# Performance work log

Measured on AMD Instinct MI355X. Metric: run time of the kernel, lower is better.

The kernel has to match this reference:

```python
import jax, jax.numpy as jnp
import numpy as np

T, B, H, D = 128, 8, 8, 64


def setup_inputs() -> dict:
    key = jax.random.key(0)
    kA, kB, kS = jax.random.split(key, 3)
    # Gated-delta transition matrices: near-identity contractions so the
    # length-T matrix-product recurrence is numerically stable, mimicking
    # A_t = gamma_t * (I - beta_t k_t k_t^T) of the gated delta rule.
    eye = jnp.eye(D, dtype=jnp.float32)
    A = 0.9 * eye + 0.06 * jax.random.normal(kA, (T, B, H, D, D), dtype=jnp.float32)
    Bm = jax.random.normal(kB, (T, B, H, D, D), dtype=jnp.float32)
    init_state = jax.random.normal(kS, (B, H, D, D), dtype=jnp.float32)
    return {"A": A, "Bm": Bm, "init_state": init_state}


def reference(A, Bm, init_state):
    """Gated delta rule recurrence S_t = S_{t-1} @ A_t + B_t for all t,
    computed with a parallel associative scan (Blelloch-equivalent).

    A:  [T,B,H,D,D] transition matrices
    Bm: [T,B,H,D,D] additive updates
    init_state: [B,H,D,D]
    returns states: [T,B,H,D,D]
    """
    def combine(e1, e2):
        # apply e1 first, then e2:
        # (S A1 + B1) A2 + B2 = S (A1 A2) + (B1 A2 + B2)
        A1, B1 = e1
        A2, B2 = e2
        A12 = jnp.einsum('tbhij,tbhjk->tbhik', A1, A2)
        B12 = jnp.einsum('tbhij,tbhjk->tbhik', B1, A2) + B2
        return (A12, B12)

    cumA, cumB = jax.lax.associative_scan(combine, (A, Bm), axis=0)
    # S_t = init_state @ cumA_t + cumB_t
    states = jnp.einsum('bhij,tbhjk->tbhik', init_state, cumA) + cumB
    return states
```

## Files before the change

kernel.cpp:

```cpp
#include <hip/hip_runtime.h>


constexpr int kT = 128;
constexpr int kBH = 64;
constexpr int kD = 64;
constexpr int kTile = kD * kD;
constexpr int kNC = 16;
constexpr int kCH = 8;

typedef __attribute__((ext_vector_type(8))) short short8;
typedef __attribute__((ext_vector_type(4))) float f32x4;
using u32 = unsigned int;

union U8 { u32 u[4]; short8 s; };

__device__ __forceinline__ void softBarrier() {
  asm volatile("s_waitcnt lgkmcnt(0)" ::: "memory");
  __builtin_amdgcn_s_barrier();
}

__device__ __forceinline__ int swzi(int r, int c) { return (r * 64 + c) ^ ((r & 7) << 3); }

__device__ __forceinline__ f32x4 mfma16(short8 a, short8 b, f32x4 c) {
  return __builtin_amdgcn_mfma_f32_16x16x32_bf16(a, b, c, 0, 0, 0);
}

__device__ __forceinline__ void pk_split(float a, float b, u32& h, u32& l) {
  u32 hu;
  asm("v_cvt_pk_bf16_f32 %0, %1, %2" : "=v"(hu) : "v"(a), "v"(b));
  const float ra = a - __uint_as_float(hu << 16);
  const float rb = b - __uint_as_float(hu & 0xffff0000u);
  u32 lu;
  asm("v_cvt_pk_bf16_f32 %0, %1, %2" : "=v"(lu) : "v"(ra), "v"(rb));
  h = hu;
  l = lu;
}

__device__ __forceinline__ short8 gather_frag(u32 p01, u32 p23, u32 q01, u32 q23,
                                              int ad0, int ad1, bool lowh) {
  U8 r;
  int x, y;
  x = __builtin_amdgcn_ds_bpermute(ad0, (int)p01);
  y = __builtin_amdgcn_ds_bpermute(ad0, (int)q01);
  r.u[0] = (u32)(lowh ? x : y);
  x = __builtin_amdgcn_ds_bpermute(ad0, (int)p23);
  y = __builtin_amdgcn_ds_bpermute(ad0, (int)q23);
  r.u[1] = (u32)(lowh ? x : y);
  x = __builtin_amdgcn_ds_bpermute(ad1, (int)p01);
  y = __builtin_amdgcn_ds_bpermute(ad1, (int)q01);
  r.u[2] = (u32)(lowh ? x : y);
  x = __builtin_amdgcn_ds_bpermute(ad1, (int)p23);
  y = __builtin_amdgcn_ds_bpermute(ad1, (int)q23);
  r.u[3] = (u32)(lowh ? x : y);
  return r.s;
}

__device__ __forceinline__ void load_pfA(float* pfA, const float* At, int lane, int w) {
#pragma unroll
  for (int kk = 0; kk < 16; ++kk) pfA[kk] = At[(w * 16 + kk) * 64 + lane];
}
__device__ __forceinline__ void load_pfB(f32x4* pfB, const float* Bt, int rowbase, int q) {
#pragma unroll
  for (int cm = 0; cm < 4; ++cm)
    pfB[cm] = *reinterpret_cast<const f32x4*>(Bt + rowbase + cm * 16 + q * 4);
}

__device__ __forceinline__ void stage_A(unsigned short* Ah, unsigned short* Al,
                                        const float* pfA, int lane, int w) {
#pragma unroll
  for (int s = 0; s < 2; ++s) {
    U8 h, l;
#pragma unroll
    for (int p = 0; p < 4; ++p) {
      u32 hu, lu;
      pk_split(pfA[s * 8 + 2 * p], pfA[s * 8 + 2 * p + 1], hu, lu);
      h.u[p] = hu;
      l.u[p] = lu;
    }
    const int idx = swzi(lane, w * 16 + s * 8);
    *reinterpret_cast<short8*>(&Ah[idx]) = h.s;
    *reinterpret_cast<short8*>(&Al[idx]) = l.s;
  }
}

__global__ __launch_bounds__(256, 4) void gdr_fold(
    const float* __restrict__ srcA, const float* __restrict__ srcB,
    float* __restrict__ dstA, float* __restrict__ dstB,
    int perChain, long chainBase, long idxBase, long elemStride, int nElem) {
  __shared__ unsigned short sAh[2][4096], sAl[2][4096];

  const int tid = threadIdx.x;
  const int lane = tid & 63, w = tid >> 6;
  const int q = lane >> 4, l15 = lane & 15;
  const int bh = blockIdx.x / perChain, id = blockIdx.x % perChain;
  const long e0 = (long)bh * chainBase + (long)id * idxBase;
  const int rowbase = (w * 16 + l15) * 64;
  const int ad0 = (l15 + ((lane >> 4) & 1) * 32) * 4;
  const int ad1 = ad0 + 64;
  const bool lowh = lane < 32;
  const int nS = nElem - 1;

  f32x4 apa[4], apb[4];
  {
    const float* At = srcA + (size_t)e0 * kTile;
    const float* Bt = srcB + (size_t)e0 * kTile;
#pragma unroll
    for (int cm = 0; cm < 4; ++cm) {
      apa[cm] = *reinterpret_cast<const f32x4*>(At + rowbase + cm * 16 + q * 4);
      apb[cm] = *reinterpret_cast<const f32x4*>(Bt + rowbase + cm * 16 + q * 4);
    }
  }

  float pfA[16];
  f32x4 pfB[4];
  load_pfA(pfA, srcA + (size_t)(e0 + elemStride) * kTile, lane, w);
  stage_A(sAh[0], sAl[0], pfA, lane, w);
  softBarrier();
  {
    const long e2 = e0 + (long)(nS > 1 ? 2 : 1) * elemStride;
    load_pfA(pfA, srcA + (size_t)e2 * kTile, lane, w);
    load_pfB(pfB, srcB + (size_t)(e0 + elemStride) * kTile, rowbase, q);
  }

  for (int j = 0; j < nS; ++j) {
    const int cur = j & 1;
    f32x4 npa[4], npb[4];
#pragma unroll
    for (int cm = 0; cm < 4; ++cm) {
      npa[cm] = (f32x4){0.f, 0.f, 0.f, 0.f};
      npb[cm] = pfB[cm];
    }
#pragma unroll
    for (int ks = 0; ks < 2; ++ks) {
      u32 pa01h, pa01l, pa23h, pa23l, qa01h, qa01l, qa23h, qa23l;
      u32 pb01h, pb01l, pb23h, pb23l, qb01h, qb01l, qb23h, qb23l;
      pk_split(apa[2 * ks][0], apa[2 * ks][1], pa01h, pa01l);
      pk_split(apa[2 * ks][2], apa[2 * ks][3], pa23h, pa23l);
      pk_split(apa[2 * ks + 1][0], apa[2 * ks + 1][1], qa01h, qa01l);
      pk_split(apa[2 * ks + 1][2], apa[2 * ks + 1][3], qa23h, qa23l);
      pk_split(apb[2 * ks][0], apb[2 * ks][1], pb01h, pb01l);
      pk_split(apb[2 * ks][2], apb[2 * ks][3], pb23h, pb23l);
      pk_split(apb[2 * ks + 1][0], apb[2 * ks + 1][1], qb01h, qb01l);
      pk_split(apb[2 * ks + 1][2], apb[2 * ks + 1][3], qb23h, qb23l);
      const short8 bah = gather_frag(pa01h, pa23h, qa01h, qa23h, ad0, ad1, lowh);
      const short8 bal = gather_frag(pa01l, pa23l, qa01l, qa23l, ad0, ad1, lowh);
      const short8 bbh = gather_frag(pb01h, pb23h, qb01h, qb23h, ad0, ad1, lowh);
      const short8 bbl = gather_frag(pb01l, pb23l, qb01l, qb23l, ad0, ad1, lowh);
#pragma unroll
      for (int cm = 0; cm < 4; ++cm) {
        const int ai = swzi(cm * 16 + l15, ks * 32 + q * 8);
        const short8 ah = *reinterpret_cast<const short8*>(&sAh[cur][ai]);
        const short8 al = *reinterpret_cast<const short8*>(&sAl[cur][ai]);
        npa[cm] = mfma16(ah, bah, npa[cm]);
        npa[cm] = mfma16(ah, bal, npa[cm]);
        npa[cm] = mfma16(al, bah, npa[cm]);
        npb[cm] = mfma16(ah, bbh, npb[cm]);
        npb[cm] = mfma16(ah, bbl, npb[cm]);
        npb[cm] = mfma16(al, bbh, npb[cm]);
      }
    }
    if (j + 1 < nS) {
      stage_A(sAh[cur ^ 1], sAl[cur ^ 1], pfA, lane, w);
      const int ja = (j + 3 <= nS) ? j + 3 : nS;
      load_pfA(pfA, srcA + (size_t)(e0 + (long)ja * elemStride) * kTile, lane, w);
      load_pfB(pfB, srcB + (size_t)(e0 + (long)(j + 2) * elemStride) * kTile, rowbase, q);
    }
#pragma unroll
    for (int cm = 0; cm < 4; ++cm) { apa[cm] = npa[cm]; apb[cm] = npb[cm]; }
    if (j + 1 < nS) softBarrier();
  }

  float* pao = dstA + (size_t)blockIdx.x * kTile;
  float* pbo = dstB + (size_t)blockIdx.x * kTile;
#pragma unroll
  for (int cm = 0; cm < 4; ++cm) {
    *reinterpret_cast<f32x4*>(pao + rowbase + cm * 16 + q * 4) = apa[cm];
    *reinterpret_cast<f32x4*>(pbo + rowbase + cm * 16 + q * 4) = apb[cm];
  }
}

__global__ __launch_bounds__(256, 4) void gdr_scan(
    const float* __restrict__ srcA, const float* __restrict__ srcB,
    const float* __restrict__ S0, float* __restrict__ out,
    int perChain, long chainBase, long idxBase, long elemStride,
    int nSteps, int tbMul, int tStep) {
  __shared__ unsigned short sAh[2][4096], sAl[2][4096];

  const int tid = threadIdx.x;
  const int lane = tid & 63, w = tid >> 6;
  const int q = lane >> 4, l15 = lane & 15;
  const int bh = blockIdx.x / perChain, id = blockIdx.x % perChain;
  const long e0 = (long)bh * chainBase + (long)id * idxBase;
  const int tBase = id * tbMul;
  const int rowbase = (w * 16 + l15) * 64;
  const int ad0 = (l15 + ((lane >> 4) & 1) * 32) * 4;
  const int ad1 = ad0 + 64;
  const bool lowh = lane < 32;

  f32x4 acc[4];
  {
    const float* Sb = (tBase == 0) ? (S0 + (size_t)bh * kTile)
                                   : (out + ((size_t)(tBase - 1) * kBH + bh) * kTile);
#pragma unroll
    for (int cm = 0; cm < 4; ++cm)
      acc[cm] = *reinterpret_cast<const f32x4*>(Sb + rowbase + cm * 16 + q * 4);
  }

  float pfA[16];
  f32x4 pfB[4];
  load_pfA(pfA, srcA + (size_t)e0 * kTile, lane, w);
  stage_A(sAh[0], sAl[0], pfA, lane, w);
  softBarrier();
  {
    const long e1 = e0 + (long)(nSteps > 1 ? 1 : 0) * elemStride;
    load_pfA(pfA, srcA + (size_t)e1 * kTile, lane, w);
    load_pfB(pfB, srcB + (size_t)e0 * kTile, rowbase, q);
  }

  for (int i = 0; i < nSteps; ++i) {
    const int cur = i & 1;
    f32x4 nacc[4];
#pragma unroll
    for (int cm = 0; cm < 4; ++cm) nacc[cm] = pfB[cm];
#pragma unroll
    for (int ks = 0; ks < 2; ++ks) {
      u32 p01h, p01l, p23h, p23l, q01h, q01l, q23h, q23l;
      pk_split(acc[2 * ks][0], acc[2 * ks][1], p01h, p01l);
      pk_split(acc[2 * ks][2], acc[2 * ks][3], p23h, p23l);
      pk_split(acc[2 * ks + 1][0], acc[2 * ks + 1][1], q01h, q01l);
      pk_split(acc[2 * ks + 1][2], acc[2 * ks + 1][3], q23h, q23l);
      const short8 bfh = gather_frag(p01h, p23h, q01h, q23h, ad0, ad1, lowh);
      const short8 bfl = gather_frag(p01l, p23l, q01l, q23l, ad0, ad1, lowh);
#pragma unroll
      for (int cm = 0; cm < 4; ++cm) {
        const int ai = swzi(cm * 16 + l15, ks * 32 + q * 8);
        const short8 ah = *reinterpret_cast<const short8*>(&sAh[cur][ai]);
        const short8 al = *reinterpret_cast<const short8*>(&sAl[cur][ai]);
        nacc[cm] = mfma16(ah, bfh, nacc[cm]);
        nacc[cm] = mfma16(ah, bfl, nacc[cm]);
        nacc[cm] = mfma16(al, bfh, nacc[cm]);
      }
    }
    if (i + 1 < nSteps) {
      stage_A(sAh[cur ^ 1], sAl[cur ^ 1], pfA, lane, w);
      const int ia = (i + 2 <= nSteps - 1) ? i + 2 : nSteps - 1;
      load_pfA(pfA, srcA + (size_t)(e0 + (long)ia * elemStride) * kTile, lane, w);
      load_pfB(pfB, srcB + (size_t)(e0 + (long)(i + 1) * elemStride) * kTile, rowbase, q);
    }
    const int t = tBase + (i + 1) * tStep - 1;
    float* o = out + ((size_t)t * kBH + bh) * kTile;
#pragma unroll
    for (int cm = 0; cm < 4; ++cm) {
      *reinterpret_cast<f32x4*>(o + rowbase + cm * 16 + q * 4) = nacc[cm];
      acc[cm] = nacc[cm];
    }
    if (i + 1 < nSteps) softBarrier();
  }
}

extern "C" void kernel_launch(void* const* d_in, const int* in_sizes, int n_in,
                              void* d_out, int out_size, void* d_ws, size_t ws_size,
                              hipStream_t stream) {
  const float* A  = (const float*)d_in[0];
  const float* Bm = (const float*)d_in[1];
  const float* S0 = (const float*)d_in[2];
  float* out = (float*)d_out;

  float* PA = (float*)d_ws;
  float* PB = PA + (size_t)kBH * kNC * kTile;

  gdr_fold<<<dim3(kBH * kNC), dim3(256), 0, stream>>>(
      A, Bm, PA, PB, kNC, 1L, (long)kCH * kBH, (long)kBH, kCH);
  gdr_scan<<<dim3(kBH), dim3(256), 0, stream>>>(
      PA, PB, S0, out, 1, (long)kNC, 0L, 1L, kNC, 0, kCH);
  gdr_scan<<<dim3(kBH * kNC), dim3(256), 0, stream>>>(
      A, Bm, S0, out, kNC, 1L, (long)kCH * kBH, (long)kBH, kCH - 1, kCH, 1);
}
```

Baseline: 152.9 us.

## Deepen A prefetch to two register buffers and issue loads before MFMA

```diff
diff --git a/kernel.cpp b/kernel.cpp
--- a/kernel.cpp
+++ b/kernel.cpp
@@ -55,33 +55,85 @@
   return r.s;
 }
 
-__device__ __forceinline__ void load_pfA(float* pfA, const float* At, int lane, int w) {
-#pragma unroll
-  for (int kk = 0; kk < 16; ++kk) pfA[kk] = At[(w * 16 + kk) * 64 + lane];
-}
-__device__ __forceinline__ void load_pfB(f32x4* pfB, const float* Bt, int rowbase, int q) {
-#pragma unroll
-  for (int cm = 0; cm < 4; ++cm)
-    pfB[cm] = *reinterpret_cast<const f32x4*>(Bt + rowbase + cm * 16 + q * 4);
-}
-
-__device__ __forceinline__ void stage_A(unsigned short* Ah, unsigned short* Al,
-                                        const float* pfA, int lane, int w) {
-#pragma unroll
-  for (int s = 0; s < 2; ++s) {
-    U8 h, l;
-#pragma unroll
-    for (int p = 0; p < 4; ++p) {
-      u32 hu, lu;
-      pk_split(pfA[s * 8 + 2 * p], pfA[s * 8 + 2 * p + 1], hu, lu);
-      h.u[p] = hu;
-      l.u[p] = lu;
-    }
-    const int idx = swzi(lane, w * 16 + s * 8);
-    *reinterpret_cast<short8*>(&Ah[idx]) = h.s;
-    *reinterpret_cast<short8*>(&Al[idx]) = l.s;
-  }
-}
+#define STAGE_A(AH, AL, BUFA)                                            \
+  do {                                                                   \
+    _Pragma("unroll") for (int s_ = 0; s_ < 2; ++s_) {                   \
+      U8 h_, l_;                                                         \
+      _Pragma("unroll") for (int p_ = 0; p_ < 4; ++p_) {                 \
+        u32 hu_, lu_;                                                    \
+        pk_split(BUFA[s_ * 8 + 2 * p_], BUFA[s_ * 8 + 2 * p_ + 1], hu_, lu_); \
+        h_.u[p_] = hu_;                                                  \
+        l_.u[p_] = lu_;                                                  \
+      }                                                                  \
+      const int idx_ = swzi(lane, w * 16 + s_ * 8);                      \
+      *reinterpret_cast<short8*>(&(AH)[idx_]) = h_.s;                    \
+      *reinterpret_cast<short8*>(&(AL)[idx_]) = l_.s;                    \
+    }                                                                    \
+  } while (0)
+
+#define LOAD_A(BUFA, ptr)                                                \
+  do {                                                                   \
+    const float* At_ = (ptr);                                            \
+    _Pragma("unroll") for (int kk_ = 0; kk_ < 16; ++kk_)                 \
+        BUFA[kk_] = At_[(w * 16 + kk_) * 64 + lane];                     \
+  } while (0)
+
+#define LOAD_B(BUFB, ptr)                                                \
+  do {                                                                   \
+    const float* Bt_ = (ptr);                                            \
+    _Pragma("unroll") for (int cm_ = 0; cm_ < 4; ++cm_)                  \
+        BUFB[cm_] = *reinterpret_cast<const f32x4*>(Bt_ + rowbase + cm_ * 16 + q * 4); \
+  } while (0)
+
+#define FOLD_STEP(J, CUR, BUFA)                                               \
+  do {                                                                        \
+    const int j_ = (J);                                                       \
+    const bool more_ = (j_ + 1 < nS);                                         \
+    f32x4 npa[4], npb[4];                                                     \
+    _Pragma("unroll") for (int cm = 0; cm < 4; ++cm) {                        \
+      npa[cm] = (f32x4){0.f, 0.f, 0.f, 0.f};                                  \
+      npb[cm] = bufB[cm];                                                     \
+    }                                                                         \
+    if (j_ + 2 <= eMax)                                                       \
+      LOAD_B(bufB, srcB + (size_t)(e0 + (long)(j_ + 2) * elemStride) * kTile);\
+    if (more_) {                                                              \
+      STAGE_A(sAh[(CUR) ^ 1], sAl[(CUR) ^ 1], BUFA);                          \
+      if (j_ + 4 <= eMax)                                                     \
+        LOAD_A(BUFA, srcA + (size_t)(e0 + (long)(j_ + 4) * elemStride) * kTile);\
+    }                                                                         \
+    _Pragma("unroll") for (int ks = 0; ks < 2; ++ks) {                        \
+      u32 pa01h, pa01l, pa23h, pa23l, qa01h, qa01l, qa23h, qa23l;             \
+      u32 pb01h, pb01l, pb23h, pb23l, qb01h, qb01l, qb23h, qb23l;             \
+      pk_split(apa[2 * ks][0], apa[2 * ks][1], pa01h, pa01l);                 \
+      pk_split(apa[2 * ks][2], apa[2 * ks][3], pa23h, pa23l);                 \
+      pk_split(apa[2 * ks + 1][0], apa[2 * ks + 1][1], qa01h, qa01l);         \
+      pk_split(apa[2 * ks + 1][2], apa[2 * ks + 1][3], qa23h, qa23l);         \
+      pk_split(apb[2 * ks][0], apb[2 * ks][1], pb01h, pb01l);                 \
+      pk_split(apb[2 * ks][2], apb[2 * ks][3], pb23h, pb23l);                 \
+      pk_split(apb[2 * ks + 1][0], apb[2 * ks + 1][1], qb01h, qb01l);         \
+      pk_split(apb[2 * ks + 1][2], apb[2 * ks + 1][3], qb23h, qb23l);         \
+      const short8 bah = gather_frag(pa01h, pa23h, qa01h, qa23h, ad0, ad1, lowh); \
+      const short8 bal = gather_frag(pa01l, pa23l, qa01l, qa23l, ad0, ad1, lowh); \
+      const short8 bbh = gather_frag(pb01h, pb23h, qb01h, qb23h, ad0, ad1, lowh); \
+      const short8 bbl = gather_frag(pb01l, pb23l, qb01l, qb23l, ad0, ad1, lowh); \
+      _Pragma("unroll") for (int cm = 0; cm < 4; ++cm) {                      \
+        const int ai = swzi(cm * 16 + l15, ks * 32 + q * 8);                  \
+        const short8 ah = *reinterpret_cast<const short8*>(&sAh[(CUR)][ai]);  \
+        const short8 al = *reinterpret_cast<const short8*>(&sAl[(CUR)][ai]);  \
+        npa[cm] = mfma16(ah, bah, npa[cm]);                                   \
+        npa[cm] = mfma16(ah, bal, npa[cm]);                                   \
+        npa[cm] = mfma16(al, bah, npa[cm]);                                   \
+        npb[cm] = mfma16(ah, bbh, npb[cm]);                                   \
+        npb[cm] = mfma16(ah, bbl, npb[cm]);                                   \
+        npb[cm] = mfma16(al, bbh, npb[cm]);                                   \
+      }                                                                       \
+    }                                                                         \
+    _Pragma("unroll") for (int cm = 0; cm < 4; ++cm) {                        \
+      apa[cm] = npa[cm];                                                      \
+      apb[cm] = npb[cm];                                                      \
+    }                                                                         \
+    if (more_) softBarrier();                                                 \
+  } while (0)
 
 __global__ __launch_bounds__(256, 4) void gdr_fold(
     const float* __restrict__ srcA, const float* __restrict__ srcB,
@@ -99,6 +151,9 @@
   const int ad1 = ad0 + 64;
   const bool lowh = lane < 32;
   const int nS = nElem - 1;
+  const int eMax = nElem - 1;
+
+  auto clampE = [&](int e) { return e < eMax ? e : eMax; };
 
   f32x4 apa[4], apb[4];
   {
@@ -111,63 +166,21 @@
     }
   }
 
-  float pfA[16];
-  f32x4 pfB[4];
-  load_pfA(pfA, srcA + (size_t)(e0 + elemStride) * kTile, lane, w);
-  stage_A(sAh[0], sAl[0], pfA, lane, w);
+  float bufA0[16], bufA1[16];
+  f32x4 bufB[4];
+  LOAD_A(bufA0, srcA + (size_t)(e0 + (long)clampE(1) * elemStride) * kTile);
+  LOAD_B(bufB, srcB + (size_t)(e0 + (long)clampE(1) * elemStride) * kTile);
+  LOAD_A(bufA1, srcA + (size_t)(e0 + (long)clampE(3) * elemStride) * kTile);
+  STAGE_A(sAh[0], sAl[0], bufA0);
+  LOAD_A(bufA0, srcA + (size_t)(e0 + (long)clampE(2) * elemStride) * kTile);
   softBarrier();
-  {
-    const long e2 = e0 + (long)(nS > 1 ? 2 : 1) * elemStride;
-    load_pfA(pfA, srcA + (size_t)e2 * kTile, lane, w);
-    load_pfB(pfB, srcB + (size_t)(e0 + elemStride) * kTile, rowbase, q);
-  }
-
-  for (int j = 0; j < nS; ++j) {
-    const int cur = j & 1;
-    f32x4 npa[4], npb[4];
-#pragma unroll
-    for (int cm = 0; cm < 4; ++cm) {
-      npa[cm] = (f32x4){0.f, 0.f, 0.f, 0.f};
-      npb[cm] = pfB[cm];
-    }
-#pragma unroll
-    for (int ks = 0; ks < 2; ++ks) {
-      u32 pa01h, pa01l, pa23h, pa23l, qa01h, qa01l, qa23h, qa23l;
-      u32 pb01h, pb01l, pb23h, pb23l, qb01h, qb01l, qb23h, qb23l;
-      pk_split(apa[2 * ks][0], apa[2 * ks][1], pa01h, pa01l);
-      pk_split(apa[2 * ks][2], apa[2 * ks][3], pa23h, pa23l);
-      pk_split(apa[2 * ks + 1][0], apa[2 * ks + 1][1], qa01h, qa01l);
-      pk_split(apa[2 * ks + 1][2], apa[2 * ks + 1][3], qa23h, qa23l);
-      pk_split(apb[2 * ks][0], apb[2 * ks][1], pb01h, pb01l);
-      pk_split(apb[2 * ks][2], apb[2 * ks][3], pb23h, pb23l);
-      pk_split(apb[2 * ks + 1][0], apb[2 * ks + 1][1], qb01h, qb01l);
-      pk_split(apb[2 * ks + 1][2], apb[2 * ks + 1][3], qb23h, qb23l);
-      const short8 bah = gather_frag(pa01h, pa23h, qa01h, qa23h, ad0, ad1, lowh);
-      const short8 bal = gather_frag(pa01l, pa23l, qa01l, qa23l, ad0, ad1, lowh);
-      const short8 bbh = gather_frag(pb01h, pb23h, qb01h, qb23h, ad0, ad1, lowh);
-      const short8 bbl = gather_frag(pb01l, pb23l, qb01l, qb23l, ad0, ad1, lowh);
-#pragma unroll
-      for (int cm = 0; cm < 4; ++cm) {
-        const int ai = swzi(cm * 16 + l15, ks * 32 + q * 8);
-        const short8 ah = *reinterpret_cast<const short8*>(&sAh[cur][ai]);
-        const short8 al = *reinterpret_cast<const short8*>(&sAl[cur][ai]);
-        npa[cm] = mfma16(ah, bah, npa[cm]);
-        npa[cm] = mfma16(ah, bal, npa[cm]);
-        npa[cm] = mfma16(al, bah, npa[cm]);
-        npb[cm] = mfma16(ah, bbh, npb[cm]);
-        npb[cm] = mfma16(ah, bbl, npb[cm]);
-        npb[cm] = mfma16(al, bbh, npb[cm]);
-      }
-    }
-    if (j + 1 < nS) {
-      stage_A(sAh[cur ^ 1], sAl[cur ^ 1], pfA, lane, w);
-      const int ja = (j + 3 <= nS) ? j + 3 : nS;
-      load_pfA(pfA, srcA + (size_t)(e0 + (long)ja * elemStride) * kTile, lane, w);
-      load_pfB(pfB, srcB + (size_t)(e0 + (long)(j + 2) * elemStride) * kTile, rowbase, q);
-    }
-#pragma unroll
-    for (int cm = 0; cm < 4; ++cm) { apa[cm] = npa[cm]; apb[cm] = npb[cm]; }
-    if (j + 1 < nS) softBarrier();
+
+  int j = 0;
+  while (true) {
+    FOLD_STEP(j, 0, bufA0);
+    if (++j >= nS) break;
+    FOLD_STEP(j, 1, bufA1);
+    if (++j >= nS) break;
   }
 
   float* pao = dstA + (size_t)blockIdx.x * kTile;
@@ -178,6 +191,45 @@
     *reinterpret_cast<f32x4*>(pbo + rowbase + cm * 16 + q * 4) = apb[cm];
   }
 }
+
+#define SCAN_STEP(I, CUR, BUFA)                                               \
+  do {                                                                        \
+    const int i_ = (I);                                                       \
+    const bool more_ = (i_ + 1 < nSteps);                                     \
+    f32x4 nacc[4];                                                            \
+    _Pragma("unroll") for (int cm = 0; cm < 4; ++cm) nacc[cm] = bufB[cm];     \
+    if (i_ + 1 <= eMax)                                                       \
+      LOAD_B(bufB, srcB + (size_t)(e0 + (long)(i_ + 1) * elemStride) * kTile);\
+    if (more_) {                                                              \
+      STAGE_A(sAh[(CUR) ^ 1], sAl[(CUR) ^ 1], BUFA);                          \
+      if (i_ + 3 <= eMax)                                                     \
+        LOAD_A(BUFA, srcA + (size_t)(e0 + (long)(i_ + 3) * elemStride) * kTile);\
+    }                                                                         \
+    _Pragma("unroll") for (int ks = 0; ks < 2; ++ks) {                        \
+      u32 p01h, p01l, p23h, p23l, q01h, q01l, q23h, q23l;                     \
+      pk_split(acc[2 * ks][0], acc[2 * ks][1], p01h, p01l);                   \
+      pk_split(acc[2 * ks][2], acc[2 * ks][3], p23h, p23l);                   \
+      pk_split(acc[2 * ks + 1][0], acc[2 * ks + 1][1], q01h, q01l);           \
+      pk_split(acc[2 * ks + 1][2], acc[2 * ks + 1][3], q23h, q23l);           \
+      const short8 bfh = gather_frag(p01h, p23h, q01h, q23h, ad0, ad1, lowh); \
+      const short8 bfl = gather_frag(p01l, p23l, q01l, q23l, ad0, ad1, lowh); \
+      _Pragma("unroll") for (int cm = 0; cm < 4; ++cm) {                      \
+        const int ai = swzi(cm * 16 + l15, ks * 32 + q * 8);                  \
+        const short8 ah = *reinterpret_cast<const short8*>(&sAh[(CUR)][ai]);  \
+        const short8 al = *reinterpret_cast<const short8*>(&sAl[(CUR)][ai]);  \
+        nacc[cm] = mfma16(ah, bfh, nacc[cm]);                                 \
+        nacc[cm] = mfma16(ah, bfl, nacc[cm]);                                 \
+        nacc[cm] = mfma16(al, bfh, nacc[cm]);                                 \
+      }                                                                       \
+    }                                                                         \
+    const int t_ = tBase + (i_ + 1) * tStep - 1;                              \
+    float* o_ = out + ((size_t)t_ * kBH + bh) * kTile;                        \
+    _Pragma("unroll") for (int cm = 0; cm < 4; ++cm) {                        \
+      *reinterpret_cast<f32x4*>(o_ + rowbase + cm * 16 + q * 4) = nacc[cm];   \
+      acc[cm] = nacc[cm];                                                     \
+    }                                                                         \
+    if (more_) softBarrier();                                                 \
+  } while (0)
 
 __global__ __launch_bounds__(256, 4) void gdr_scan(
     const float* __restrict__ srcA, const float* __restrict__ srcB,
@@ -196,6 +248,9 @@
   const int ad0 = (l15 + ((lane >> 4) & 1) * 32) * 4;
   const int ad1 = ad0 + 64;
   const bool lowh = lane < 32;
+  const int eMax = nSteps - 1;
+
+  auto clampE = [&](int e) { return e < eMax ? e : eMax; };
 
   f32x4 acc[4];
   {
@@ -206,55 +261,21 @@
       acc[cm] = *reinterpret_cast<const f32x4*>(Sb + rowbase + cm * 16 + q * 4);
   }
 
-  float pfA[16];
-  f32x4 pfB[4];
-  load_pfA(pfA, srcA + (size_t)e0 * kTile, lane, w);
-  stage_A(sAh[0], sAl[0], pfA, lane, w);
+  float bufA0[16], bufA1[16];
+  f32x4 bufB[4];
+  LOAD_A(bufA0, srcA + (size_t)e0 * kTile);
+  LOAD_B(bufB, srcB + (size_t)e0 * kTile);
+  LOAD_A(bufA1, srcA + (size_t)(e0 + (long)clampE(2) * elemStride) * kTile);
+  STAGE_A(sAh[0], sAl[0], bufA0);
+  LOAD_A(bufA0, srcA + (size_t)(e0 + (long)clampE(1) * elemStride) * kTile);
   softBarrier();
-  {
-    const long e1 = e0 + (long)(nSteps > 1 ? 1 : 0) * elemStride;
-    load_pfA(pfA, srcA + (size_t)e1 * kTile, lane, w);
-    load_pfB(pfB, srcB + (size_t)e0 * kTile, rowbase, q);
-  }
-
-  for (int i = 0; i < nSteps; ++i) {
-    const int cur = i & 1;
-    f32x4 nacc[4];
-#pragma unroll
-    for (int cm = 0; cm < 4; ++cm) nacc[cm] = pfB[cm];
-#pragma unroll
-    for (int ks = 0; ks < 2; ++ks) {
-      u32 p01h, p01l, p23h, p23l, q01h, q01l, q23h, q23l;
-      pk_split(acc[2 * ks][0], acc[2 * ks][1], p01h, p01l);
-      pk_split(acc[2 * ks][2], acc[2 * ks][3], p23h, p23l);
-      pk_split(acc[2 * ks + 1][0], acc[2 * ks + 1][1], q01h, q01l);
-      pk_split(acc[2 * ks + 1][2], acc[2 * ks + 1][3], q23h, q23l);
-      const short8 bfh = gather_frag(p01h, p23h, q01h, q23h, ad0, ad1, lowh);
-      const short8 bfl = gather_frag(p01l, p23l, q01l, q23l, ad0, ad1, lowh);
-#pragma unroll
-      for (int cm = 0; cm < 4; ++cm) {
-        const int ai = swzi(cm * 16 + l15, ks * 32 + q * 8);
-        const short8 ah = *reinterpret_cast<const short8*>(&sAh[cur][ai]);
-        const short8 al = *reinterpret_cast<const short8*>(&sAl[cur][ai]);
-        nacc[cm] = mfma16(ah, bfh, nacc[cm]);
-        nacc[cm] = mfma16(ah, bfl, nacc[cm]);
-        nacc[cm] = mfma16(al, bfh, nacc[cm]);
-      }
-    }
-    if (i + 1 < nSteps) {
-      stage_A(sAh[cur ^ 1], sAl[cur ^ 1], pfA, lane, w);
-      const int ia = (i + 2 <= nSteps - 1) ? i + 2 : nSteps - 1;
-      load_pfA(pfA, srcA + (size_t)(e0 + (long)ia * elemStride) * kTile, lane, w);
-      load_pfB(pfB, srcB + (size_t)(e0 + (long)(i + 1) * elemStride) * kTile, rowbase, q);
-    }
-    const int t = tBase + (i + 1) * tStep - 1;
-    float* o = out + ((size_t)t * kBH + bh) * kTile;
-#pragma unroll
-    for (int cm = 0; cm < 4; ++cm) {
-      *reinterpret_cast<f32x4*>(o + rowbase + cm * 16 + q * 4) = nacc[cm];
-      acc[cm] = nacc[cm];
-    }
-    if (i + 1 < nSteps) softBarrier();
+
+  int i = 0;
+  while (true) {
+    SCAN_STEP(i, 0, bufA0);
+    if (++i >= nSteps) break;
+    SCAN_STEP(i, 1, bufA1);
+    if (++i >= nSteps) break;
   }
 }
 
```

New measurement: 185.8 us. +21.6%, slower.
